# Kernel tuning notes

Hardware: AMD Instinct MI355X
Metric: run time of the kernel (lower is better)

## Reference

```python
import jax, jax.numpy as jnp
import numpy as np

DIM_X, DIM_Z, D_MODEL, N_HEADS, BATCH = 512, 256, 256, 8, 32


def sinusoidal_pe(seq_len, d_model):
    # standard sinusoidal table, rows indexed by position
    pos = np.arange(seq_len)[:, None].astype(np.float32)
    div = np.exp(np.arange(0, d_model, 2).astype(np.float32) * (-np.log(10000.0) / d_model))
    pe = np.zeros((seq_len, d_model), dtype=np.float32)
    pe[:, 0::2] = np.sin(pos * div)
    pe[:, 1::2] = np.cos(pos * div)
    return jnp.asarray(pe)


def setup_inputs() -> dict:
    key = jax.random.key(0)
    ks = jax.random.split(key, 5)
    state = jax.random.normal(ks[0], (BATCH, D_MODEL, DIM_X), dtype=jnp.float32)
    obs = jax.random.normal(ks[1], (BATCH, D_MODEL, DIM_Z), dtype=jnp.float32)
    Qp = jax.random.uniform(ks[2], (DIM_X, D_MODEL), dtype=jnp.float32)  # torch.rand init
    Wq = jax.random.normal(ks[3], (D_MODEL, D_MODEL), dtype=jnp.float32) / np.sqrt(D_MODEL)
    Wk = jax.random.normal(ks[4], (D_MODEL, D_MODEL), dtype=jnp.float32) / np.sqrt(D_MODEL)
    bq = jnp.zeros((D_MODEL,), dtype=jnp.float32)
    bk = jnp.zeros((D_MODEL,), dtype=jnp.float32)
    return {"state": state, "obs": obs, "Qp": Qp, "Wq": Wq, "bq": bq, "Wk": Wk, "bk": bk}


def reference(state, obs, Qp, Wq, bq, Wk, bk):
    bs, en, dim_x = state.shape
    dim_z = obs.shape[2]
    d_model = Qp.shape[1]
    h = N_HEADS
    hd = d_model // h
    S = dim_x + dim_z

    # mean-center over the ensemble axis
    A = state - jnp.mean(state, axis=1, keepdims=True)   # [bs, en, dim_x]
    Y = obs - jnp.mean(obs, axis=1, keepdims=True)       # [bs, en, dim_z]
    A = jnp.transpose(A, (2, 0, 1))                      # [dim_x, bs, en]
    Y = jnp.transpose(Y, (2, 0, 1))                      # [dim_z, bs, en]

    # positional encoding: batch_first=True quirk -> PE indexed along axis 1 (the bs axis)
    pe = sinusoidal_pe(bs, d_model)[None, :, :]          # [1, bs, d_model]
    query = Qp[:, None, :] + pe                          # [dim_x, bs, d_model] (broadcast of repeat)
    xy = jnp.concatenate([A, Y], axis=0) + pe            # [S, bs, d_model]

    # multi-head attention weights (V / out-proj do not affect returned quantities)
    q = (query @ Wq.T + bq).reshape(dim_x, bs, h, hd)
    k = (xy @ Wk.T + bk).reshape(S, bs, h, hd)
    scores = jnp.einsum('lbhd,sbhd->bhls', q, k) / np.sqrt(hd)  # [bs, h, dim_x, S]

    # fixed structured mask: eye(dim_x) | bottom-padded eye(dim_z)
    p1 = jnp.eye(dim_x, dtype=bool)
    p2 = jnp.concatenate([jnp.zeros((dim_x - dim_z, dim_z), dtype=bool),
                          jnp.eye(dim_z, dtype=bool)], axis=0)
    allow = jnp.concatenate([p1, p2], axis=1)            # [dim_x, S]
    scores = jnp.where(allow[None, None], scores, -jnp.inf)
    atten = jnp.mean(jax.nn.softmax(scores, axis=-1), axis=1)  # average over heads -> [bs, dim_x, S]

    # weighted merge of the ORIGINAL (uncentered) state/obs
    merge = jnp.concatenate([jnp.transpose(state, (0, 2, 1)),
                             jnp.transpose(obs, (0, 2, 1))], axis=1)  # [bs, S, en]
    new_state = jnp.einsum('bls,bse->ble', atten, merge)              # [bs, dim_x, en]
    new_state = jnp.transpose(new_state, (0, 2, 1))                   # [bs, en, dim_x]
    return new_state, atten
```

## Files before the change

kernel.cpp:

```cpp
#include <hip/hip_runtime.h>
#include <stdint.h>
#include <math.h>


#define WS_P    0
#define WS_QWT  8192
#define WS_PQ   73728
#define WS_U    81920
#define WS_V    606208
#define WS_QPT  671744
#define WS_WQT  737280

typedef float vf4 __attribute__((ext_vector_type(4)));
__device__ __forceinline__ void nt_store4(float* p, float x, float y,
                                          float z, float w) {
  vf4 v; v.x = x; v.y = y; v.z = z; v.w = w;
  __builtin_nontemporal_store(v, (vf4*)p);
}

__global__ void __launch_bounds__(256)
k_tr(const float* __restrict__ Qp, const float* __restrict__ Wq,
     float* __restrict__ ws) {
  __shared__ float tile[32][33];
  int bid = blockIdx.x, t = threadIdx.x;
  const float* src; float* dst; int ti;
  if (bid < 64) { src = Qp + 65536; dst = ws + WS_QPT; ti = bid; }
  else          { src = Wq;         dst = ws + WS_WQT; ti = bid - 64; }
  int tr = ti >> 3, tc = ti & 7;
  int c = t & 31, r0 = t >> 5;
  #pragma unroll
  for (int k = 0; k < 4; ++k) {
    int r = r0 + (k << 3);
    tile[r][c] = src[(size_t)(tr * 32 + r) * 256 + tc * 32 + c];
  }
  __syncthreads();
  #pragma unroll
  for (int k = 0; k < 4; ++k) {
    int r = r0 + (k << 3);
    dst[(size_t)(tc * 32 + r) * 256 + tr * 32 + c] = tile[c][r];
  }
}

__global__ void __launch_bounds__(256)
k_pro(const float* __restrict__ Wq, float* __restrict__ ws) {
  int bid = blockIdx.x, t = threadIdx.x;
  __shared__ float lvec[256];
  const float* __restrict__ GT; float* dst;
  if (bid < 256) {
    int d = bid;
    lvec[t] = Wq[(size_t)d * 256 + t];
    GT = ws + WS_QPT; dst = ws + WS_QWT + d * 256;
  } else {
    int b = bid - 256;
    int k2 = t & ~1;
    float div = expf((float)k2 * (-9.210340371976184f / 256.f));
    float a = (float)b * div;
    lvec[t] = (t & 1) ? cosf(a) : sinf(a);
    GT = ws + WS_WQT; dst = ws + WS_PQ + b * 256;
  }
  __syncthreads();
  float acc = 0.f;
  #pragma unroll 8
  for (int e = 0; e < 256; ++e)
    acc += lvec[e] * GT[(e << 8) + t];
  dst[t] = acc;
}

__global__ void __launch_bounds__(256)
k_uv(const float* __restrict__ Wk, const float* __restrict__ bq,
     float* __restrict__ ws) {
  int bid = blockIdx.x, t = threadIdx.x;
  if (bid < 256) {
    int h = bid >> 5, e0 = (bid & 31) << 3;
    __shared__ float wk_s[32][9];
    {
      int d = t >> 3, i = t & 7;
      wk_s[d][i] = Wk[(size_t)(h * 32 + d) * 256 + e0 + i];
    }
    __syncthreads();
    float acc[8] = {0.f, 0.f, 0.f, 0.f, 0.f, 0.f, 0.f, 0.f};
    const float* __restrict__ Qw = ws + WS_QWT + t;
    #pragma unroll 4
    for (int d = 0; d < 32; ++d) {
      float q = Qw[((h << 5) + d) << 8];
      #pragma unroll
      for (int i = 0; i < 8; ++i) acc[i] += wk_s[d][i] * q;
    }
    float* Uh = ws + WS_U + (h << 16) + (size_t)e0 * 256;
    #pragma unroll
    for (int i = 0; i < 8; ++i) Uh[(size_t)i * 256 + t] = acc[i];
  } else {
    int idx = bid - 256, b = idx >> 3, h = idx & 7;
    float acc = 0.f;
#pragma unroll 8
    for (int dd = 0; dd < 32; ++dd) {
      int d = h * 32 + dd;
      acc += (ws[WS_PQ + b * 256 + d] + bq[d]) * Wk[(size_t)d * 256 + t];
    }
    ws[WS_V + ((b << 3) + h) * 256 + t] = acc;
  }
}

__global__ void __launch_bounds__(256)
k_delta(const float* __restrict__ state, const float* __restrict__ obs,
        float* __restrict__ ws) {
  int b = blockIdx.x >> 3, jt = (blockIdx.x & 7) << 5;
  int t = threadIdx.x;
  __shared__ float Xs[256][33];
  __shared__ float Vs[2048];
  __shared__ float pd[8][8][32];
  __shared__ float pw[8][8][32];
  __shared__ float px[8][32];
  {
    int es = t >> 3, jq = t & 7;
    const float* sp = state + (size_t)b * 131072 + 256 + jt + (jq << 2);
    const float* op = obs   + (size_t)b * 65536  + jt + (jq << 2);
    #pragma unroll
    for (int k = 0; k < 8; ++k) {
      int e = es + (k << 5);
      float4 s4 = *(const float4*)(sp + (size_t)e * 512);
      float4 o4 = *(const float4*)(op + (size_t)e * 256);
      float* xr = &Xs[e][jq << 2];
      xr[0] = s4.x - o4.x; xr[1] = s4.y - o4.y;
      xr[2] = s4.z - o4.z; xr[3] = s4.w - o4.w;
    }
    for (int i = t; i < 2048; i += 256) Vs[i] = ws[WS_V + (b << 11) + i];
  }
  __syncthreads();
  int j = t & 31, eg = t >> 5, e0 = eg << 5;
  {
    float ax = 0.f;
    #pragma unroll
    for (int ei = 0; ei < 32; ++ei) ax += Xs[e0 + ei][j];
    px[eg][j] = ax;
  }
  const float* __restrict__ Ub = ws + WS_U + jt + j;
  #pragma unroll
  for (int h = 0; h < 8; ++h) {
    float dacc = 0.f, wacc = 0.f;
    const float* __restrict__ Uh = Ub + (h << 16) + (e0 << 8);
    const float* __restrict__ Vh = Vs + (h << 8) + e0;
    #pragma unroll 16
    for (int ei = 0; ei < 32; ++ei) {
      float w = Uh[ei << 8] + Vh[ei];
      dacc += Xs[e0 + ei][j] * w;
      wacc += w;
    }
    pd[eg][h][j] = dacc;
    pw[eg][h][j] = wacc;
  }
  __syncthreads();
  int h2 = t >> 5, j2 = t & 31;
  float D = 0.f, W = 0.f, X = 0.f;
  #pragma unroll
  for (int g = 0; g < 8; ++g) {
    D += pd[g][h2][j2];
    W += pw[g][h2][j2];
    X += px[g][j2];
  }
  float delta = D - X * (1.f / 256.f) * W;
  float sig = 1.f / (1.f + __expf(-delta * 0.17677669529663687f));
  __syncthreads();
  px[h2][j2] = sig;
  __syncthreads();
  if (t < 32) {
    float acc = 0.f;
    #pragma unroll
    for (int h = 0; h < 8; ++h) acc += px[h][t];
    ws[WS_P + (b << 8) + jt + t] = acc;
  }
}

__global__ void __launch_bounds__(256)
k_out(const float* __restrict__ state, const float* __restrict__ obs,
      const float* __restrict__ ws, float* __restrict__ out) {
  int bid = blockIdx.x, t = threadIdx.x;
  if (bid < 4096) {
    int row = (bid << 1) | (t >> 7);
    int tt = t & 127;
    int b = row >> 8;
    float4 sv = ((const float4*)(state + (size_t)row * 512))[tt];
    float* wrow = out + (size_t)row * 512 + (tt << 2);
    if (tt < 64) {
      nt_store4(wrow, sv.x, sv.y, sv.z, sv.w);
    } else {
      float4 ov = ((const float4*)(obs + (size_t)row * 256))[tt - 64];
      float4 p4 = ((const float4*)(ws + WS_P + b * 256))[tt - 64];
      p4.x *= 0.125f; p4.y *= 0.125f; p4.z *= 0.125f; p4.w *= 0.125f;
      nt_store4(wrow,
                p4.x * sv.x + (1.f - p4.x) * ov.x,
                p4.y * sv.y + (1.f - p4.y) * ov.y,
                p4.z * sv.z + (1.f - p4.z) * ov.z,
                p4.w * sv.w + (1.f - p4.w) * ov.w);
    }
  } else {
    int g4 = (bid - 4096) * 256 + t;
    int r = g4 / 192, c = g4 - r * 192;
    int b = r >> 9, l = r & 511;
    int s0 = c << 2;
    float v[4] = {0.f, 0.f, 0.f, 0.f};
    if (l < 256) {
      if (l >= s0 && l < s0 + 4) v[l - s0] = 1.0f;
    } else {
      float p = ws[WS_P + b * 256 + (l - 256)] * 0.125f;
      if (l >= s0 && l < s0 + 4) v[l - s0] = p;
      int s2 = l + 256;
      if (s2 >= s0 && s2 < s0 + 4) v[s2 - s0] = 1.0f - p;
    }
    nt_store4(out + 4194304 + ((size_t)g4 << 2), v[0], v[1], v[2], v[3]);
  }
}

extern "C" void kernel_launch(void* const* d_in, const int* in_sizes, int n_in,
                              void* d_out, int out_size, void* d_ws, size_t ws_size,
                              hipStream_t stream) {
  const float *state = nullptr, *obs = nullptr, *Qp = nullptr;
  const float *Wq = nullptr, *Wk = nullptr, *bq = nullptr, *bk = nullptr;
  for (int i = 0; i < n_in; ++i) {
    int s = in_sizes[i];
    const float* p = (const float*)d_in[i];
    if      (s == 4194304) state = p;
    else if (s == 2097152) obs = p;
    else if (s == 131072)  Qp = p;
    else if (s == 65536)   { if (!Wq) Wq = p; else Wk = p; }
    else if (s == 256)     { if (!bq) bq = p; else bk = p; }
  }
  (void)bk;
  float* out = (float*)d_out;
  float* ws  = (float*)d_ws;

  k_tr   <<<128,   256, 0, stream>>>(Qp, Wq, ws);
  k_pro  <<<288,   256, 0, stream>>>(Wq, ws);
  k_uv   <<<512,   256, 0, stream>>>(Wk, bq, ws);
  k_delta<<<256,   256, 0, stream>>>(state, obs, ws);
  k_out  <<<16384, 256, 0, stream>>>(state, obs, ws, out);
}
```

Before: 126.6 us.

## Spread output writes that do not depend on attention across earlier small kernels

The output stores that do not depend on the computed attention probabilities (the identity and zero parts of the attention matrix, and the copied first half of each state row) now run as extra blocks in the early setup kernels. Those kernels previously launched only a few hundred blocks. The final kernel is left with only the blend of the second half and the two probability entries per row. The aim is to fill otherwise idle GPU capacity during the small prologue kernels and shrink the bandwidth-bound tail. The early kernels get larger grids, and the write traffic is divided differently across launches.

After: 126.7 us. About the same (+0.1%).

```diff
diff --git a/kernel.cpp b/kernel.cpp
--- a/kernel.cpp
+++ b/kernel.cpp
@@ -20,55 +20,84 @@
 
 __global__ void __launch_bounds__(256)
 k_tr(const float* __restrict__ Qp, const float* __restrict__ Wq,
-     float* __restrict__ ws) {
-  __shared__ float tile[32][33];
-  int bid = blockIdx.x, t = threadIdx.x;
-  const float* src; float* dst; int ti;
-  if (bid < 64) { src = Qp + 65536; dst = ws + WS_QPT; ti = bid; }
-  else          { src = Wq;         dst = ws + WS_WQT; ti = bid - 64; }
-  int tr = ti >> 3, tc = ti & 7;
-  int c = t & 31, r0 = t >> 5;
-  #pragma unroll
-  for (int k = 0; k < 4; ++k) {
-    int r = r0 + (k << 3);
-    tile[r][c] = src[(size_t)(tr * 32 + r) * 256 + tc * 32 + c];
-  }
-  __syncthreads();
-  #pragma unroll
-  for (int k = 0; k < 4; ++k) {
-    int r = r0 + (k << 3);
-    dst[(size_t)(tc * 32 + r) * 256 + tr * 32 + c] = tile[c][r];
-  }
-}
-
-__global__ void __launch_bounds__(256)
-k_pro(const float* __restrict__ Wq, float* __restrict__ ws) {
-  int bid = blockIdx.x, t = threadIdx.x;
-  __shared__ float lvec[256];
-  const float* __restrict__ GT; float* dst;
-  if (bid < 256) {
-    int d = bid;
-    lvec[t] = Wq[(size_t)d * 256 + t];
-    GT = ws + WS_QPT; dst = ws + WS_QWT + d * 256;
-  } else {
-    int b = bid - 256;
-    int k2 = t & ~1;
-    float div = expf((float)k2 * (-9.210340371976184f / 256.f));
-    float a = (float)b * div;
-    lvec[t] = (t & 1) ? cosf(a) : sinf(a);
-    GT = ws + WS_WQT; dst = ws + WS_PQ + b * 256;
-  }
-  __syncthreads();
-  float acc = 0.f;
-  #pragma unroll 8
-  for (int e = 0; e < 256; ++e)
-    acc += lvec[e] * GT[(e << 8) + t];
-  dst[t] = acc;
+     float* __restrict__ ws, float* __restrict__ out) {
+  int bid = blockIdx.x, t = threadIdx.x;
+  if (bid < 128) {
+    __shared__ float tile[32][33];
+    const float* src; float* dst; int ti;
+    if (bid < 64) { src = Qp + 65536; dst = ws + WS_QPT; ti = bid; }
+    else          { src = Wq;         dst = ws + WS_WQT; ti = bid - 64; }
+    int tr = ti >> 3, tc = ti & 7;
+    int c = t & 31, r0 = t >> 5;
+    #pragma unroll
+    for (int k = 0; k < 4; ++k) {
+      int r = r0 + (k << 3);
+      tile[r][c] = src[(size_t)(tr * 32 + r) * 256 + tc * 32 + c];
+    }
+    __syncthreads();
+    #pragma unroll
+    for (int k = 0; k < 4; ++k) {
+      int r = r0 + (k << 3);
+      dst[(size_t)(tc * 32 + r) * 256 + tr * 32 + c] = tile[c][r];
+    }
+  } else {
+    int base = (bid - 128) * 512 + t;
+    #pragma unroll
+    for (int k = 0; k < 2; ++k) {
+      int g4 = base + (k << 8);
+      int row_id = g4 / 192, c = g4 - row_id * 192;
+      int b = row_id >> 8, l = row_id & 255;
+      float v[4] = {0.f, 0.f, 0.f, 0.f};
+      int s0 = c << 2;
+      if (l >= s0 && l < s0 + 4) v[l - s0] = 1.0f;
+      nt_store4(out + 4194304 + (size_t)((b << 9) + l) * 768 + (c << 2),
+                v[0], v[1], v[2], v[3]);
+    }
+  }
+}
+
+__global__ void __launch_bounds__(256)
+k_pro(const float* __restrict__ Wq, float* __restrict__ ws,
+      float* __restrict__ out) {
+  int bid = blockIdx.x, t = threadIdx.x;
+  if (bid < 288) {
+    __shared__ float lvec[256];
+    const float* __restrict__ GT; float* dst;
+    if (bid < 256) {
+      int d = bid;
+      lvec[t] = Wq[(size_t)d * 256 + t];
+      GT = ws + WS_QPT; dst = ws + WS_QWT + d * 256;
+    } else {
+      int b = bid - 256;
+      int k2 = t & ~1;
+      float div = expf((float)k2 * (-9.210340371976184f / 256.f));
+      float a = (float)b * div;
+      lvec[t] = (t & 1) ? cosf(a) : sinf(a);
+      GT = ws + WS_WQT; dst = ws + WS_PQ + b * 256;
+    }
+    __syncthreads();
+    float acc = 0.f;
+    #pragma unroll 8
+    for (int e = 0; e < 256; ++e)
+      acc += lvec[e] * GT[(e << 8) + t];
+    dst[t] = acc;
+  } else {
+    int base = (bid - 288) * 512 + t;
+    #pragma unroll
+    for (int k = 0; k < 2; ++k) {
+      int g4 = base + (k << 8);
+      int row_id = g4 / 192, c = g4 - row_id * 192;
+      int b = row_id >> 8, l = 256 + (row_id & 255);
+      nt_store4(out + 4194304 + (size_t)((b << 9) + l) * 768 + (c << 2),
+                0.f, 0.f, 0.f, 0.f);
+    }
+  }
 }
 
 __global__ void __launch_bounds__(256)
 k_uv(const float* __restrict__ Wk, const float* __restrict__ bq,
-     float* __restrict__ ws) {
+     const float* __restrict__ state, float* __restrict__ ws,
+     float* __restrict__ out) {
   int bid = blockIdx.x, t = threadIdx.x;
   if (bid < 256) {
     int h = bid >> 5, e0 = (bid & 31) << 3;
@@ -89,7 +118,7 @@
     float* Uh = ws + WS_U + (h << 16) + (size_t)e0 * 256;
     #pragma unroll
     for (int i = 0; i < 8; ++i) Uh[(size_t)i * 256 + t] = acc[i];
-  } else {
+  } else if (bid < 512) {
     int idx = bid - 256, b = idx >> 3, h = idx & 7;
     float acc = 0.f;
 #pragma unroll 8
@@ -98,6 +127,15 @@
       acc += (ws[WS_PQ + b * 256 + d] + bq[d]) * Wk[(size_t)d * 256 + t];
     }
     ws[WS_V + ((b << 3) + h) * 256 + t] = acc;
+  } else {
+    int base = (bid - 512) * 512 + t;
+    #pragma unroll
+    for (int k = 0; k < 2; ++k) {
+      int g4 = base + (k << 8);
+      int row = g4 >> 6, c = g4 & 63;
+      float4 sv = ((const float4*)state)[(size_t)row * 128 + c];
+      nt_store4(out + (size_t)row * 512 + (c << 2), sv.x, sv.y, sv.z, sv.w);
+    }
   }
 }
 
@@ -175,39 +213,26 @@
 k_out(const float* __restrict__ state, const float* __restrict__ obs,
       const float* __restrict__ ws, float* __restrict__ out) {
   int bid = blockIdx.x, t = threadIdx.x;
-  if (bid < 4096) {
-    int row = (bid << 1) | (t >> 7);
-    int tt = t & 127;
+  if (bid < 2048) {
+    int row = (bid << 2) | (t >> 6);
+    int c = t & 63;
     int b = row >> 8;
-    float4 sv = ((const float4*)(state + (size_t)row * 512))[tt];
-    float* wrow = out + (size_t)row * 512 + (tt << 2);
-    if (tt < 64) {
-      nt_store4(wrow, sv.x, sv.y, sv.z, sv.w);
-    } else {
-      float4 ov = ((const float4*)(obs + (size_t)row * 256))[tt - 64];
-      float4 p4 = ((const float4*)(ws + WS_P + b * 256))[tt - 64];
-      p4.x *= 0.125f; p4.y *= 0.125f; p4.z *= 0.125f; p4.w *= 0.125f;
-      nt_store4(wrow,
-                p4.x * sv.x + (1.f - p4.x) * ov.x,
-                p4.y * sv.y + (1.f - p4.y) * ov.y,
-                p4.z * sv.z + (1.f - p4.z) * ov.z,
-                p4.w * sv.w + (1.f - p4.w) * ov.w);
-    }
-  } else {
-    int g4 = (bid - 4096) * 256 + t;
-    int r = g4 / 192, c = g4 - r * 192;
-    int b = r >> 9, l = r & 511;
-    int s0 = c << 2;
-    float v[4] = {0.f, 0.f, 0.f, 0.f};
-    if (l < 256) {
-      if (l >= s0 && l < s0 + 4) v[l - s0] = 1.0f;
-    } else {
-      float p = ws[WS_P + b * 256 + (l - 256)] * 0.125f;
-      if (l >= s0 && l < s0 + 4) v[l - s0] = p;
-      int s2 = l + 256;
-      if (s2 >= s0 && s2 < s0 + 4) v[s2 - s0] = 1.0f - p;
-    }
-    nt_store4(out + 4194304 + ((size_t)g4 << 2), v[0], v[1], v[2], v[3]);
+    float4 sv = ((const float4*)(state + (size_t)row * 512))[64 + c];
+    float4 ov = ((const float4*)(obs + (size_t)row * 256))[c];
+    float4 p4 = ((const float4*)(ws + WS_P + b * 256))[c];
+    p4.x *= 0.125f; p4.y *= 0.125f; p4.z *= 0.125f; p4.w *= 0.125f;
+    nt_store4(out + (size_t)row * 512 + 256 + (c << 2),
+              p4.x * sv.x + (1.f - p4.x) * ov.x,
+              p4.y * sv.y + (1.f - p4.y) * ov.y,
+              p4.z * sv.z + (1.f - p4.z) * ov.z,
+              p4.w * sv.w + (1.f - p4.w) * ov.w);
+  } else {
+    int idx = ((bid - 2048) << 8) + t;
+    int b = idx >> 8, j = idx & 255;
+    float p = ws[WS_P + (b << 8) + j] * 0.125f;
+    size_t r = 4194304 + (size_t)((b << 9) + 256 + j) * 768;
+    out[r + 256 + j] = p;
+    out[r + 512 + j] = 1.f - p;
   }
 }
 
@@ -229,9 +254,9 @@
   float* out = (float*)d_out;
   float* ws  = (float*)d_ws;
 
-  k_tr   <<<128,   256, 0, stream>>>(Qp, Wq, ws);
-  k_pro  <<<288,   256, 0, stream>>>(Wq, ws);
-  k_uv   <<<512,   256, 0, stream>>>(Wk, bq, ws);
-  k_delta<<<256,   256, 0, stream>>>(state, obs, ws);
-  k_out  <<<16384, 256, 0, stream>>>(state, obs, ws, out);
-}
+  k_tr   <<<3200, 256, 0, stream>>>(Qp, Wq, ws, out);
+  k_pro  <<<3360, 256, 0, stream>>>(Wq, ws, out);
+  k_uv   <<<1536, 256, 0, stream>>>(Wk, bq, state, ws, out);
+  k_delta<<<256,  256, 0, stream>>>(state, obs, ws);
+  k_out  <<<2080, 256, 0, stream>>>(state, obs, ws, out);
+}
```

## Fuse new_state blend for observed columns into k_delta using shared state-obs diff

Applied to the files above, without the earlier changes.

k_delta already holds state-minus-obs for its 32 columns in shared memory. It now also writes the blended output for the last 256 state columns directly as obs + p*(state-obs), so state no longer has to be re-read for those columns. k_out shrinks to copying the first 256 state columns plus writing the attention matrix. This saves one read of state's second half and one launch-side pass. The cost is that the small 256-block k_delta does more serial store work and gets a longer tail.

Result: no change. 125.1 us (-1.2%).

```diff
diff --git a/kernel.cpp b/kernel.cpp
--- a/kernel.cpp
+++ b/kernel.cpp
@@ -103,7 +103,7 @@
 
 __global__ void __launch_bounds__(256)
 k_delta(const float* __restrict__ state, const float* __restrict__ obs,
-        float* __restrict__ ws) {
+        float* __restrict__ ws, float* __restrict__ out) {
   int b = blockIdx.x >> 3, jt = (blockIdx.x & 7) << 5;
   int t = threadIdx.x;
   __shared__ float Xs[256][33];
@@ -111,6 +111,7 @@
   __shared__ float pd[8][8][32];
   __shared__ float pw[8][8][32];
   __shared__ float px[8][32];
+  __shared__ float pfin[32];
   {
     int es = t >> 3, jq = t & 7;
     const float* sp = state + (size_t)b * 131072 + 256 + jt + (jq << 2);
@@ -168,33 +169,37 @@
     #pragma unroll
     for (int h = 0; h < 8; ++h) acc += px[h][t];
     ws[WS_P + (b << 8) + jt + t] = acc;
-  }
-}
-
-__global__ void __launch_bounds__(256)
-k_out(const float* __restrict__ state, const float* __restrict__ obs,
-      const float* __restrict__ ws, float* __restrict__ out) {
-  int bid = blockIdx.x, t = threadIdx.x;
-  if (bid < 4096) {
-    int row = (bid << 1) | (t >> 7);
-    int tt = t & 127;
-    int b = row >> 8;
-    float4 sv = ((const float4*)(state + (size_t)row * 512))[tt];
-    float* wrow = out + (size_t)row * 512 + (tt << 2);
-    if (tt < 64) {
-      nt_store4(wrow, sv.x, sv.y, sv.z, sv.w);
-    } else {
-      float4 ov = ((const float4*)(obs + (size_t)row * 256))[tt - 64];
-      float4 p4 = ((const float4*)(ws + WS_P + b * 256))[tt - 64];
-      p4.x *= 0.125f; p4.y *= 0.125f; p4.z *= 0.125f; p4.w *= 0.125f;
-      nt_store4(wrow,
-                p4.x * sv.x + (1.f - p4.x) * ov.x,
-                p4.y * sv.y + (1.f - p4.y) * ov.y,
-                p4.z * sv.z + (1.f - p4.z) * ov.z,
-                p4.w * sv.w + (1.f - p4.w) * ov.w);
-    }
+    pfin[t] = acc * 0.125f;
+  }
+  __syncthreads();
+  {
+    int eb = t >> 3, j0 = (t & 7) << 2;
+    const float* op2 = obs + (size_t)b * 65536 + jt + j0;
+    float p0 = pfin[j0], p1 = pfin[j0 + 1], p2 = pfin[j0 + 2], p3 = pfin[j0 + 3];
+    float* orow = out + (size_t)b * 131072 + 256 + jt + j0;
+    #pragma unroll
+    for (int k = 0; k < 8; ++k) {
+      int e = eb + (k << 5);
+      float4 o4 = *(const float4*)(op2 + (size_t)e * 256);
+      const float* xr = &Xs[e][j0];
+      nt_store4(orow + (size_t)e * 512,
+                o4.x + p0 * xr[0], o4.y + p1 * xr[1],
+                o4.z + p2 * xr[2], o4.w + p3 * xr[3]);
+    }
+  }
+}
+
+__global__ void __launch_bounds__(256)
+k_out(const float* __restrict__ state, const float* __restrict__ ws,
+      float* __restrict__ out) {
+  int bid = blockIdx.x, t = threadIdx.x;
+  if (bid < 2048) {
+    int row = (bid << 2) | (t >> 6);
+    int c = t & 63;
+    float4 sv = ((const float4*)(state + (size_t)row * 512))[c];
+    nt_store4(out + (size_t)row * 512 + (c << 2), sv.x, sv.y, sv.z, sv.w);
   } else {
-    int g4 = (bid - 4096) * 256 + t;
+    int g4 = (bid - 2048) * 256 + t;
     int r = g4 / 192, c = g4 - r * 192;
     int b = r >> 9, l = r & 511;
     int s0 = c << 2;
@@ -232,6 +237,6 @@
   k_tr   <<<128,   256, 0, stream>>>(Qp, Wq, ws);
   k_pro  <<<288,   256, 0, stream>>>(Wq, ws);
   k_uv   <<<512,   256, 0, stream>>>(Wk, bq, ws);
-  k_delta<<<256,   256, 0, stream>>>(state, obs, ws);
-  k_out  <<<16384, 256, 0, stream>>>(state, obs, ws, out);
-}
+  k_delta<<<256,   256, 0, stream>>>(state, obs, ws, out);
+  k_out  <<<14336, 256, 0, stream>>>(state, ws, out);
+}
```
